# Kernel optimization log

Measured on AMD Instinct MI355X. Metric: run time of the kernel, lower is better.

Reference implementation:

```python
import jax, jax.numpy as jnp
import numpy as np

T = 0.12  # softmax temperature


def _mlp(x, Wa, ba, Wb, bb, Wc, bc):
    # Linear -> ReLU -> (Dropout=id in eval) -> Linear -> ReLU -> Linear -> ReLU
    h = jax.nn.relu(x @ Wa + ba)
    h = jax.nn.relu(h @ Wb + bb)
    return jax.nn.relu(h @ Wc + bc)


def setup_inputs() -> dict:
    key = jax.random.key(0)
    ks = jax.random.split(key, 16)
    B, K, A, P = 2048, 64, 312, 128
    std = 0.01  # torch init: normal(0, 0.01), bias 0
    inp = {
        "v2s": jax.random.normal(ks[0], (B, A), jnp.float32),
        "tar_atts": jax.random.uniform(ks[1], (B, 1), jnp.float32),
        "sample_indices": jax.random.randint(ks[2], (B, K), 0, B),
        # CLproject[1]: 1 -> 1024 -> 2048 -> 312
        "W2a": std * jax.random.normal(ks[3], (1, 1024), jnp.float32),
        "b2a": jnp.zeros((1024,), jnp.float32),
        "W2b": std * jax.random.normal(ks[4], (1024, 2048), jnp.float32),
        "b2b": jnp.zeros((2048,), jnp.float32),
        "W2c": std * jax.random.normal(ks[5], (2048, A), jnp.float32),
        "b2c": jnp.zeros((A,), jnp.float32),
        # CLproject[0]: 312 -> 1024 -> 2048 -> 128
        "W1a": std * jax.random.normal(ks[6], (A, 1024), jnp.float32),
        "b1a": jnp.zeros((1024,), jnp.float32),
        "W1b": std * jax.random.normal(ks[7], (1024, 2048), jnp.float32),
        "b1b": jnp.zeros((2048,), jnp.float32),
        "W1c": std * jax.random.normal(ks[8], (2048, P), jnp.float32),
        "b1c": jnp.zeros((P,), jnp.float32),
    }
    return inp


def reference(v2s, tar_atts, sample_indices, W2a, b2a, W2b, b2b, W2c, b2c,
              W1a, b1a, W1b, b1b, W1c, b1c):
    # attribute embedding via CLproject[1]: [B,1] -> [B,312]
    att = _mlp(tar_atts, W2a, b2a, W2b, b2b, W2c, b2c)
    v2s_sg = jax.lax.stop_gradient(v2s)  # detach().clone()
    # gather padded pos+neg sample lists: [B,K,312]
    samples = v2s_sg[sample_indices]
    # per-sample projection via CLproject[0]
    proj_samples = _mlp(samples + att[:, None, :], W1a, b1a, W1b, b1b, W1c, b1c)  # [B,K,128]
    query = _mlp(v2s_sg + att, W1a, b1a, W1b, b1b, W1c, b1c)  # [B,128]
    # batched version of per-sample einsum('c,kc->k')
    logits = jnp.einsum("bc,bkc->bk", query, proj_samples) / T
    return logits
```

## Files before the change

kernel.cpp:

```cpp
#include <hip/hip_runtime.h>
#include <stdio.h>
#include <stdint.h>

typedef __attribute__((ext_vector_type(8))) short short8;
typedef __attribute__((ext_vector_type(4))) float f32x4;
typedef __attribute__((ext_vector_type(4))) unsigned short ushort4v;

__device__ __forceinline__ unsigned short f2bf(float f) {
  unsigned int u = __builtin_bit_cast(unsigned int, f);
  u = u + 0x7FFFu + ((u >> 16) & 1u);
  return (unsigned short)(u >> 16);
}
__device__ __forceinline__ float bf2f(unsigned short h) {
  unsigned int u = ((unsigned int)h) << 16;
  return __builtin_bit_cast(float, u);
}

__device__ __forceinline__ void gl_lds16(const unsigned short* g, unsigned short* l) {
  __builtin_amdgcn_global_load_lds(
      (const __attribute__((address_space(1))) unsigned int*)(const void*)g,
      (__attribute__((address_space(3))) unsigned int*)(void*)l, 16, 0, 0);
}

__global__ void k_transpose_cast(const float* __restrict__ in, unsigned short* __restrict__ out,
                                 int Nin, int Kin, int ldo) {
  int k = blockIdx.x * blockDim.x + threadIdx.x;
  int n = blockIdx.y;
  if (k >= ldo) return;
  float v = (n < Nin && k < Kin) ? in[(size_t)k * Nin + n] : 0.f;
  out[(size_t)n * ldo + k] = f2bf(v);
}

__global__ void k_att_l1(const float* __restrict__ tar, const float* __restrict__ W2a,
                         const float* __restrict__ b2a, unsigned short* __restrict__ out) {
  int id = blockIdx.x * 256 + threadIdx.x;
  int b = id >> 10, j = id & 1023;
  out[id] = f2bf(fmaxf(tar[b] * W2a[j] + b2a[j], 0.f));
}

__global__ void k_v2s_cast(const float* __restrict__ v2s, unsigned short* __restrict__ out) {
  int id = blockIdx.x * 256 + threadIdx.x;
  int r = id / 320, c = id - r * 320;
  out[id] = (c < 312) ? f2bf(v2s[(size_t)r * 312 + c]) : (unsigned short)0;
}

__device__ __forceinline__ int lds_off(int row, int g) {
  int slot = (g + (row >> 1)) & 3;
  return row * 32 + slot * 8;
}

template<bool RELU, bool OUTBF16>
__global__ __launch_bounds__(256)
void k_gemm_bt(const unsigned short* __restrict__ A, const unsigned short* __restrict__ B,
               const float* __restrict__ bias, int bias_n, int nNt, int N_store, int K,
               void* __restrict__ outp, int ldo, int remap) {
  __shared__ __align__(16) unsigned short As[128 * 32];
  __shared__ __align__(16) unsigned short Bs[128 * 32];
  int d = blockIdx.x, nwg = gridDim.x;
  int L = d;
  if (remap) { int q = nwg >> 3; L = (d & 7) * q + (d >> 3); }
  int mt = L / nNt, nt = L - mt * nNt;
  size_t m0 = (size_t)mt * 128, n0 = (size_t)nt * 128;
  int tid = threadIdx.x, lane = tid & 63;
  int w = tid >> 6, wr = w >> 1, wc = w & 1;
  int sr = tid >> 2;
  int gch = ((tid & 3) - (tid >> 3)) & 3;
  const unsigned short* pA0 = A + (m0 + sr) * K + gch * 8;
  const unsigned short* pA1 = pA0 + (size_t)64 * K;
  const unsigned short* pB0 = B + (n0 + sr) * K + gch * 8;
  const unsigned short* pB1 = pB0 + (size_t)64 * K;
  unsigned short* lA0 = &As[(tid & ~63) * 8];
  unsigned short* lA1 = &As[64 * 32 + (tid & ~63) * 8];
  unsigned short* lB0 = &Bs[(tid & ~63) * 8];
  unsigned short* lB1 = &Bs[64 * 32 + (tid & ~63) * 8];

  int kg = lane >> 4, l15 = lane & 15;
  int aoff = lds_off(wr * 64 + l15, kg);
  int boff = lds_off(wc * 64 + l15, kg);

  f32x4 acc[4][4];
  #pragma unroll
  for (int i = 0; i < 4; ++i)
    #pragma unroll
    for (int j = 0; j < 4; ++j) acc[i][j] = (f32x4)(0.f);

  for (int k0 = 0; k0 < K; k0 += 32) {
    __syncthreads();
    gl_lds16(pA0 + k0, lA0);
    gl_lds16(pA1 + k0, lA1);
    gl_lds16(pB0 + k0, lB0);
    gl_lds16(pB1 + k0, lB1);
    __syncthreads();
    short8 af[4], bfr[4];
    #pragma unroll
    for (int mi = 0; mi < 4; ++mi) af[mi] = *(const short8*)&As[aoff + mi * 512];
    #pragma unroll
    for (int ni = 0; ni < 4; ++ni) bfr[ni] = *(const short8*)&Bs[boff + ni * 512];
    #pragma unroll
    for (int mi = 0; mi < 4; ++mi)
      #pragma unroll
      for (int ni = 0; ni < 4; ++ni)
        acc[mi][ni] = __builtin_amdgcn_mfma_f32_16x16x32_bf16(af[mi], bfr[ni], acc[mi][ni], 0, 0, 0);
  }

  #pragma unroll
  for (int ni = 0; ni < 4; ++ni) {
    int colg = (int)n0 + wc * 64 + ni * 16 + l15;
    if (colg < N_store) {
      float bs = bias ? (colg < bias_n ? bias[colg] : 0.f) : 0.f;
      #pragma unroll
      for (int mi = 0; mi < 4; ++mi) {
        #pragma unroll
        for (int r2 = 0; r2 < 4; ++r2) {
          size_t rowg = m0 + wr * 64 + mi * 16 + kg * 4 + r2;
          float v = acc[mi][ni][r2] + bs;
          if (RELU) v = fmaxf(v, 0.f);
          if (OUTBF16) ((unsigned short*)outp)[rowg * ldo + colg] = f2bf(v);
          else         ((float*)outp)[rowg * ldo + colg] = v;
        }
      }
    }
  }
}

__global__ void k_build_h1(const float* __restrict__ V1, const float* __restrict__ A1p,
                           const int* __restrict__ idx, unsigned short* __restrict__ H1c,
                           int rbase) {
  int row = rbase + blockIdx.x;
  int src, arow;
  if (row < 2048) { src = row; arow = row; }
  else {
    int g = row - 2048; arow = g >> 6;
    int s = idx[g];
    src = s < 0 ? 0 : (s > 2047 ? 2047 : s);
  }
  int j = threadIdx.x * 4;
  float4 v = *(const float4*)(V1 + (size_t)src * 1024 + j);
  float4 a = *(const float4*)(A1p + (size_t)arow * 1024 + j);
  ushort4v o;
  o.x = f2bf(fmaxf(v.x + a.x, 0.f));
  o.y = f2bf(fmaxf(v.y + a.y, 0.f));
  o.z = f2bf(fmaxf(v.z + a.z, 0.f));
  o.w = f2bf(fmaxf(v.w + a.w, 0.f));
  *(ushort4v*)(H1c + (size_t)blockIdx.x * 1024 + j) = o;
}

__global__ void k_dot(const unsigned short* __restrict__ P, float* __restrict__ out) {
  __shared__ float q[128];
  int b = blockIdx.x, t = threadIdx.x;
  if (t < 128) q[t] = bf2f(P[(size_t)b * 128 + t]);
  __syncthreads();
  int k = t >> 2, part = t & 3;
  const unsigned short* row = P + (size_t)(2048 + b * 64 + k) * 128 + part * 32;
  const float* qp = q + part * 32;
  float s = 0.f;
  #pragma unroll
  for (int j = 0; j < 32; j += 8) {
    short8 pv = *(const short8*)(row + j);
    #pragma unroll
    for (int e = 0; e < 8; ++e)
      s += bf2f((unsigned short)pv[e]) * qp[j + e];
  }
  s += __shfl_xor(s, 1);
  s += __shfl_xor(s, 2);
  if (part == 0) out[(size_t)b * 64 + k] = s * (float)(1.0 / 0.12);
}

extern "C" void kernel_launch(void* const* d_in, const int* in_sizes, int n_in,
                              void* d_out, int out_size, void* d_ws, size_t ws_size,
                              hipStream_t stream) {
  const float* v2s = (const float*)d_in[0];
  const float* tar = (const float*)d_in[1];
  const int*   sidx = (const int*)d_in[2];
  const float* W2a = (const float*)d_in[3];
  const float* b2a = (const float*)d_in[4];
  const float* W2b = (const float*)d_in[5];
  const float* b2b = (const float*)d_in[6];
  const float* W2c = (const float*)d_in[7];
  const float* b2c = (const float*)d_in[8];
  const float* W1a = (const float*)d_in[9];
  const float* b1a = (const float*)d_in[10];
  const float* W1b = (const float*)d_in[11];
  const float* b1b = (const float*)d_in[12];
  const float* W1c = (const float*)d_in[13];
  const float* b1c = (const float*)d_in[14];
  float* out = (float*)d_out;

  char* ws = (char*)d_ws;
  size_t off = 0;
  auto alloc = [&](size_t bytes) -> char* {
    char* p = ws + off; off += (bytes + 255) & ~(size_t)255; return p;
  };
  unsigned short* W1bT = (unsigned short*)alloc(2048ull * 1024 * 2);
  unsigned short* W1cT = (unsigned short*)alloc(128ull * 2048 * 2);
  float*          V1   = (float*)alloc(2048ull * 1024 * 4);
  float*          A1p  = (float*)alloc(2048ull * 1024 * 4);
  unsigned short* Pb   = (unsigned short*)alloc(133120ull * 128 * 2);
  size_t O = off;
  off = O;
  unsigned short* W1aT = (unsigned short*)alloc(1024ull * 320 * 2);
  unsigned short* v2sb = (unsigned short*)alloc(2048ull * 320 * 2);
  unsigned short* attb = (unsigned short*)alloc(2048ull * 320 * 2);
  unsigned short* W2bT = (unsigned short*)alloc(2048ull * 1024 * 2);
  unsigned short* W2cT = (unsigned short*)alloc(384ull * 2048 * 2);
  unsigned short* h_a  = (unsigned short*)alloc(2048ull * 1024 * 2);
  unsigned short* h2a  = (unsigned short*)alloc(2048ull * 2048 * 2);
  size_t early_end = off;

  const int cands[5] = {1, 2, 4, 8, 16};
  int NCH = -1, R = 0;
  size_t needed = 0;
  for (int ci = 0; ci < 5; ++ci) {
    int c = cands[ci];
    size_t Rr = 133120ull / c;
    size_t late = O + (((Rr * 1024 * 2) + 255) & ~(size_t)255)
                    + (((Rr * 2048 * 2) + 255) & ~(size_t)255);
    size_t need = late > early_end ? late : early_end;
    if (need <= ws_size) { NCH = c; R = (int)Rr; needed = need; break; }
  }
  fprintf(stderr, "[kernel_launch] ws_size=%zu NCH=%d needed=%zu\n", ws_size, NCH, needed);
  if (NCH < 0) {
    hipMemsetAsync(d_out, 0, (size_t)out_size * 4, stream);
    return;
  }
  off = O;
  unsigned short* H1c = (unsigned short*)alloc((size_t)R * 1024 * 2);
  unsigned short* H2c = (unsigned short*)alloc((size_t)R * 2048 * 2);

  dim3 blk(256);
  k_transpose_cast<<<dim3(4, 2048), blk, 0, stream>>>(W2b, W2bT, 2048, 1024, 1024);
  k_transpose_cast<<<dim3(8, 384),  blk, 0, stream>>>(W2c, W2cT, 312, 2048, 2048);
  k_transpose_cast<<<dim3(2, 1024), blk, 0, stream>>>(W1a, W1aT, 1024, 312, 320);
  k_transpose_cast<<<dim3(4, 2048), blk, 0, stream>>>(W1b, W1bT, 2048, 1024, 1024);
  k_transpose_cast<<<dim3(8, 128),  blk, 0, stream>>>(W1c, W1cT, 128, 2048, 2048);
  k_att_l1<<<8192, blk, 0, stream>>>(tar, W2a, b2a, h_a);
  k_v2s_cast<<<2560, blk, 0, stream>>>(v2s, v2sb);
  k_gemm_bt<true,  true ><<<256, blk, 0, stream>>>(h_a,  W2bT, b2b, 2048, 16, 2048, 1024, h2a,  2048, 1);
  k_gemm_bt<true,  true ><<<48,  blk, 0, stream>>>(h2a,  W2cT, b2c, 312,  3,  320,  2048, attb, 320,  1);
  k_gemm_bt<false, false><<<128, blk, 0, stream>>>(v2sb, W1aT, nullptr, 0,  8, 1024, 320, V1,  1024, 1);
  k_gemm_bt<false, false><<<128, blk, 0, stream>>>(attb, W1aT, b1a, 1024,  8, 1024, 320, A1p, 1024, 1);
  for (int c = 0; c < NCH; ++c) {
    int rbase = c * R;
    k_build_h1<<<R, blk, 0, stream>>>(V1, A1p, sidx, H1c, rbase);
    k_gemm_bt<true, true><<<(R / 128) * 16, blk, 0, stream>>>(H1c, W1bT, b1b, 2048, 16, 2048, 1024, H2c, 2048, 1);
    k_gemm_bt<true, true><<<(R / 128), blk, 0, stream>>>(H2c, W1cT, b1c, 128, 1, 128, 2048,
                                                          Pb + (size_t)rbase * 128, 128, 0);
  }
  k_dot<<<2048, blk, 0, stream>>>(Pb, out);
}
```

Measured before the change: 1.173 ms.

## Add 256x256-tile triple-buffered GEMM for the dominant per-sample hidden layer

Adds a new 512-thread bf16 MFMA GEMM kernel with 256x256 output tiles, a three-stage global-to-LDS pipeline via direct global_load_lds, and raised wave priority around the MFMA block. It replaces the 128x128 GEMM for the large 1024->2048 layer over the 133k gathered sample rows whenever the workspace allows at most 8 chunks. Bigger tiles are meant to double operand reuse per LDS load and reduce global traffic, while the deeper prefetch hides load latency. The cost is higher register and LDS pressure (128 accumulator floats per thread, 96KB LDS) and fewer resident workgroups.

```diff
diff --git a/kernel.cpp b/kernel.cpp
--- a/kernel.cpp
+++ b/kernel.cpp
@@ -20,6 +20,11 @@
   __builtin_amdgcn_global_load_lds(
       (const __attribute__((address_space(1))) unsigned int*)(const void*)g,
       (__attribute__((address_space(3))) unsigned int*)(void*)l, 16, 0, 0);
+}
+
+__device__ __forceinline__ int lds_off(int row, int g) {
+  int slot = (g + (row >> 1)) & 3;
+  return row * 32 + slot * 8;
 }
 
 __global__ void k_transpose_cast(const float* __restrict__ in, unsigned short* __restrict__ out,
@@ -44,9 +49,91 @@
   out[id] = (c < 312) ? f2bf(v2s[(size_t)r * 312 + c]) : (unsigned short)0;
 }
 
-__device__ __forceinline__ int lds_off(int row, int g) {
-  int slot = (g + (row >> 1)) & 3;
-  return row * 32 + slot * 8;
+__global__ __launch_bounds__(512, 2)
+void k_gemm256(const unsigned short* __restrict__ A, const unsigned short* __restrict__ B,
+               const float* __restrict__ bias, int nNt, int K,
+               unsigned short* __restrict__ outp, int ldo) {
+  __shared__ __align__(16) unsigned short sm[3 * 16384];
+  int d = blockIdx.x, nwg = gridDim.x;
+  int q = nwg >> 3;
+  int L = (d & 7) * q + (d >> 3);
+  int mt = L / nNt, nt = L - mt * nNt;
+  size_t m0 = (size_t)mt * 256, n0 = (size_t)nt * 256;
+  int tid = threadIdx.x, lane = tid & 63;
+  int w = tid >> 6, wr = w >> 2, wc = w & 3;
+  int r0 = tid >> 2;
+  int gch = ((tid & 3) - (tid >> 3)) & 3;
+  const unsigned short* Asrc0 = A + (m0 + r0) * K + gch * 8;
+  const unsigned short* Asrc1 = A + (m0 + r0 + 128) * K + gch * 8;
+  const unsigned short* Bsrc0 = B + (n0 + r0) * K + gch * 8;
+  const unsigned short* Bsrc1 = B + (n0 + r0 + 128) * K + gch * 8;
+  int ldst0 = w * 512;
+  int ldst1 = 4096 + w * 512;
+
+#define STAGE(t_, b_) do {                                              \
+    int k0_ = (t_) * 32;                                                \
+    unsigned short* Ab_ = &sm[(b_) * 16384];                            \
+    unsigned short* Bb_ = &sm[(b_) * 16384 + 8192];                     \
+    gl_lds16(Asrc0 + k0_, Ab_ + ldst0);                                 \
+    gl_lds16(Asrc1 + k0_, Ab_ + ldst1);                                 \
+    gl_lds16(Bsrc0 + k0_, Bb_ + ldst0);                                 \
+    gl_lds16(Bsrc1 + k0_, Bb_ + ldst1);                                 \
+  } while (0)
+
+  int kg = lane >> 4, l15 = lane & 15;
+  int aoff = lds_off(wr * 128 + l15, kg);
+  int boff = lds_off(wc * 64 + l15, kg);
+
+  f32x4 acc[8][4];
+  #pragma unroll
+  for (int i = 0; i < 8; ++i)
+    #pragma unroll
+    for (int j = 0; j < 4; ++j) acc[i][j] = (f32x4)(0.f);
+
+  const int NT = K >> 5;
+  STAGE(0, 0);
+  STAGE(1, 1);
+  asm volatile("s_waitcnt vmcnt(4)" ::: "memory");
+  __syncthreads();
+
+  for (int t = 0; t < NT; ++t) {
+    int cur = t % 3;
+    if (t + 2 < NT) STAGE(t + 2, (t + 2) % 3);
+    const unsigned short* Ab = &sm[cur * 16384];
+    const unsigned short* Bb = &sm[cur * 16384 + 8192];
+    short8 af[8], bfv[4];
+    #pragma unroll
+    for (int mi = 0; mi < 8; ++mi) af[mi] = *(const short8*)&Ab[aoff + mi * 512];
+    #pragma unroll
+    for (int ni = 0; ni < 4; ++ni) bfv[ni] = *(const short8*)&Bb[boff + ni * 512];
+    __builtin_amdgcn_s_setprio(1);
+    #pragma unroll
+    for (int mi = 0; mi < 8; ++mi)
+      #pragma unroll
+      for (int ni = 0; ni < 4; ++ni)
+        acc[mi][ni] = __builtin_amdgcn_mfma_f32_16x16x32_bf16(af[mi], bfv[ni], acc[mi][ni], 0, 0, 0);
+    __builtin_amdgcn_s_setprio(0);
+    if (t + 1 < NT) {
+      if (t + 2 < NT) asm volatile("s_waitcnt vmcnt(4)" ::: "memory");
+      else            asm volatile("s_waitcnt vmcnt(0)" ::: "memory");
+      __syncthreads();
+    }
+  }
+#undef STAGE
+
+  #pragma unroll
+  for (int ni = 0; ni < 4; ++ni) {
+    int colg = (int)n0 + wc * 64 + ni * 16 + l15;
+    float bs = bias[colg];
+    #pragma unroll
+    for (int mi = 0; mi < 8; ++mi) {
+      #pragma unroll
+      for (int r2 = 0; r2 < 4; ++r2) {
+        size_t rowg = m0 + wr * 128 + mi * 16 + kg * 4 + r2;
+        outp[rowg * ldo + colg] = f2bf(fmaxf(acc[mi][ni][r2] + bs, 0.f));
+      }
+    }
+  }
 }
 
 template<bool RELU, bool OUTBF16>
@@ -207,18 +294,25 @@
   unsigned short* h2a  = (unsigned short*)alloc(2048ull * 2048 * 2);
   size_t early_end = off;
 
-  const int cands[5] = {1, 2, 4, 8, 16};
+  const int cands[4] = {1, 2, 4, 8};
   int NCH = -1, R = 0;
-  size_t needed = 0;
-  for (int ci = 0; ci < 5; ++ci) {
+  for (int ci = 0; ci < 4; ++ci) {
     int c = cands[ci];
     size_t Rr = 133120ull / c;
     size_t late = O + (((Rr * 1024 * 2) + 255) & ~(size_t)255)
                     + (((Rr * 2048 * 2) + 255) & ~(size_t)255);
     size_t need = late > early_end ? late : early_end;
-    if (need <= ws_size) { NCH = c; R = (int)Rr; needed = need; break; }
-  }
-  fprintf(stderr, "[kernel_launch] ws_size=%zu NCH=%d needed=%zu\n", ws_size, NCH, needed);
+    if (need <= ws_size) { NCH = c; R = (int)Rr; break; }
+  }
+  int use256 = (NCH > 0);
+  if (NCH < 0) {
+    size_t Rr = 133120ull / 16;
+    size_t late = O + (((Rr * 1024 * 2) + 255) & ~(size_t)255)
+                    + (((Rr * 2048 * 2) + 255) & ~(size_t)255);
+    size_t need = late > early_end ? late : early_end;
+    if (need <= ws_size) { NCH = 16; R = (int)Rr; }
+  }
+  fprintf(stderr, "[kernel_launch] ws_size=%zu NCH=%d use256=%d\n", ws_size, NCH, use256);
   if (NCH < 0) {
     hipMemsetAsync(d_out, 0, (size_t)out_size * 4, stream);
     return;
@@ -242,7 +336,10 @@
   for (int c = 0; c < NCH; ++c) {
     int rbase = c * R;
     k_build_h1<<<R, blk, 0, stream>>>(V1, A1p, sidx, H1c, rbase);
-    k_gemm_bt<true, true><<<(R / 128) * 16, blk, 0, stream>>>(H1c, W1bT, b1b, 2048, 16, 2048, 1024, H2c, 2048, 1);
+    if (use256)
+      k_gemm256<<<(R / 256) * 8, dim3(512), 0, stream>>>(H1c, W1bT, b1b, 8, 1024, H2c, 2048);
+    else
+      k_gemm_bt<true, true><<<(R / 128) * 16, blk, 0, stream>>>(H1c, W1bT, b1b, 2048, 16, 2048, 1024, H2c, 2048, 1);
     k_gemm_bt<true, true><<<(R / 128), blk, 0, stream>>>(H2c, W1cT, b1c, 128, 1, 128, 2048,
                                                           Pb + (size_t)rbase * 128, 128, 0);
   }
```

Result: no change. 1.166 ms (-0.6%).
